# Optimization experiments

Hardware: AMD Instinct MI355X
Metric: run time of the kernel (lower is better)

The kernel has to match this reference:

```python
import jax, jax.numpy as jnp
import numpy as np

D = 256; DFFN = 1024; H = 8; NLVL = 4; NPNT = 4; HD = D // H
BS = 4; NQ = 100; NPTS = 25
SPATIAL = [(128, 128), (64, 64), (32, 32), (16, 16)]
LEN_IN = sum(h * w for h, w in SPATIAL)


def _ln(x, g, b, eps=1e-5):
    m = x.mean(-1, keepdims=True)
    v = ((x - m) ** 2).mean(-1, keepdims=True)
    return (x - m) * jax.lax.rsqrt(v + eps) * g + b


def _mha(q, k, v, w_in, b_in, w_out, b_out):
    # torch nn.MultiheadAttention math, batch-first layout [B,S,D]
    B, Sq, _ = q.shape; Sk = k.shape[1]
    wq, wk, wv = jnp.split(w_in, 3, 0); bq, bk, bv = jnp.split(b_in, 3)
    qh = (q @ wq.T + bq).reshape(B, Sq, H, HD).transpose(0, 2, 1, 3)
    kh = (k @ wk.T + bk).reshape(B, Sk, H, HD).transpose(0, 2, 1, 3)
    vh = (v @ wv.T + bv).reshape(B, Sk, H, HD).transpose(0, 2, 1, 3)
    a = jax.nn.softmax(jnp.einsum('bhqd,bhkd->bhqk', qh, kh) * (1.0 / float(np.sqrt(HD))), -1)
    o = jnp.einsum('bhqk,bhkd->bhqd', a, vh).transpose(0, 2, 1, 3).reshape(B, Sq, D)
    return o @ w_out.T + b_out


def _msdeform(query, ref, src, off_w, off_b, aw_w, aw_b, val_w, val_b, out_w, out_b):
    # MSDeformAttn: per-query multi-level bilinear sampling + weighted aggregation
    bs, Lq, _ = query.shape
    value = (src @ val_w.T + val_b).reshape(bs, LEN_IN, H, HD)
    off = (query @ off_w.T + off_b).reshape(bs, Lq, H, NLVL, NPNT, 2)
    aw = jax.nn.softmax((query @ aw_w.T + aw_b).reshape(bs, Lq, H, NLVL * NPNT), -1)
    aw = aw.reshape(bs, Lq, H, NLVL, NPNT)
    norm = jnp.array([[w, h] for h, w in SPATIAL], jnp.float32)  # (W,H) per level
    loc = ref[:, :, None, :, None, :] + off / norm[None, None, None, :, None, :]
    out = jnp.zeros((bs, H, Lq, HD), query.dtype)
    start = 0
    for l, (hh, ww) in enumerate(SPATIAL):
        v_l = value[:, start:start + hh * ww].transpose(0, 2, 1, 3)  # [bs,H,hw,HD]
        start += hh * ww
        # grid_sample align_corners=False pixel coords: loc*size - 0.5
        x = (loc[:, :, :, l, :, 0] * ww - 0.5).transpose(0, 2, 1, 3).reshape(bs, H, Lq * NPNT)
        y = (loc[:, :, :, l, :, 1] * hh - 0.5).transpose(0, 2, 1, 3).reshape(bs, H, Lq * NPNT)
        x0 = jnp.floor(x); y0 = jnp.floor(y); wx = x - x0; wy = y - y0
        x0i = x0.astype(jnp.int32); y0i = y0.astype(jnp.int32); x1i = x0i + 1; y1i = y0i + 1
        def g(xi, yi):
            valid = ((xi >= 0) & (xi < ww) & (yi >= 0) & (yi < hh)).astype(query.dtype)
            idx = jnp.clip(yi, 0, hh - 1) * ww + jnp.clip(xi, 0, ww - 1)
            return jnp.take_along_axis(v_l, idx[..., None], axis=2) * valid[..., None]
        s = (g(x0i, y0i) * ((1 - wx) * (1 - wy))[..., None]
             + g(x1i, y0i) * (wx * (1 - wy))[..., None]
             + g(x0i, y1i) * ((1 - wx) * wy)[..., None]
             + g(x1i, y1i) * (wx * wy)[..., None])
        s = s.reshape(bs, H, Lq, NPNT, HD)
        out = out + (s * aw[:, :, :, l].transpose(0, 2, 1, 3)[..., None]).sum(3)
    return out.transpose(0, 2, 1, 3).reshape(bs, Lq, D) @ out_w.T + out_b


def _fwd(tgt, query_pos, reference_points, src,
         w_in_intra, b_in_intra, w_out_intra, b_out_intra, g_norm_intra, b_norm_intra,
         w_in_inter, b_in_inter, w_out_inter, b_out_inter, g_norm_inter, b_norm_inter,
         off_w, off_b, aw_w, aw_b, val_w, val_b, co_w, co_b, g_norm_cross, b_norm_cross,
         lin1_w, lin1_b, lin2_w, lin2_b, g_norm3, b_norm3):
    bs, nq, npts, d = tgt.shape
    # intra-instance self-attention (over control points)
    q = (tgt + query_pos).reshape(bs * nq, npts, d)
    t2 = _mha(q, q, tgt.reshape(bs * nq, npts, d), w_in_intra, b_in_intra, w_out_intra, b_out_intra)
    tgt = _ln(tgt + t2.reshape(bs, nq, npts, d), g_norm_intra, b_norm_intra)
    # inter-instance self-attention (over queries), no pos embed per source code
    ti = tgt.transpose(0, 2, 1, 3).reshape(bs * npts, nq, d)
    t2 = _mha(ti, ti, ti, w_in_inter, b_in_inter, w_out_inter, b_out_inter)
    ti = _ln(ti + t2, g_norm_inter, b_norm_inter).reshape(bs, npts, nq, d).transpose(0, 2, 1, 3)
    # deformable cross-attention
    ref = jnp.broadcast_to(reference_points[:, :, None], (bs, nq, npts, NLVL, 2)).reshape(bs, nq * npts, NLVL, 2)
    qc = (ti + query_pos).reshape(bs, nq * npts, d)
    t2 = _msdeform(qc, ref, src, off_w, off_b, aw_w, aw_b, val_w, val_b, co_w, co_b).reshape(bs, nq, npts, d)
    tgt = _ln(ti + t2, g_norm_cross, b_norm_cross)
    # FFN
    ff = jax.nn.relu(tgt @ lin1_w.T + lin1_b) @ lin2_w.T + lin2_b
    return _ln(tgt + ff, g_norm3, b_norm3)


def setup_inputs() -> dict:
    key = jax.random.key(0)
    ki = iter(jax.random.split(key, 40))
    def rn(shape, sc=0.02):
        return jax.random.normal(next(ki), shape, jnp.float32) * sc
    inp = dict(
        tgt=jax.random.normal(next(ki), (BS, NQ, NPTS, D), jnp.float32),
        query_pos=jax.random.normal(next(ki), (BS, NQ, NPTS, D), jnp.float32),
        reference_points=jax.random.uniform(next(ki), (BS, NQ, NLVL, 2), jnp.float32),
        src=jax.random.normal(next(ki), (BS, LEN_IN, D), jnp.float32),
        w_in_intra=rn((3 * D, D)), b_in_intra=jnp.zeros((3 * D,), jnp.float32),
        w_out_intra=rn((D, D)), b_out_intra=jnp.zeros((D,), jnp.float32),
        g_norm_intra=jnp.ones((D,), jnp.float32), b_norm_intra=jnp.zeros((D,), jnp.float32),
        w_in_inter=rn((3 * D, D)), b_in_inter=jnp.zeros((3 * D,), jnp.float32),
        w_out_inter=rn((D, D)), b_out_inter=jnp.zeros((D,), jnp.float32),
        g_norm_inter=jnp.ones((D,), jnp.float32), b_norm_inter=jnp.zeros((D,), jnp.float32),
        off_w=rn((H * NLVL * NPNT * 2, D), 0.001), off_b=rn((H * NLVL * NPNT * 2,), 0.5),
        aw_w=rn((H * NLVL * NPNT, D)), aw_b=jnp.zeros((H * NLVL * NPNT,), jnp.float32),
        val_w=rn((D, D)), val_b=jnp.zeros((D,), jnp.float32),
        co_w=rn((D, D)), co_b=jnp.zeros((D,), jnp.float32),
        g_norm_cross=jnp.ones((D,), jnp.float32), b_norm_cross=jnp.zeros((D,), jnp.float32),
        lin1_w=rn((DFFN, D)), lin1_b=jnp.zeros((DFFN,), jnp.float32),
        lin2_w=rn((D, DFFN)), lin2_b=jnp.zeros((D,), jnp.float32),
        g_norm3=jnp.ones((D,), jnp.float32), b_norm3=jnp.zeros((D,), jnp.float32),
        src_spatial_shapes=jnp.array(SPATIAL, jnp.int32),
        level_start_index=jnp.array(np.cumsum([0] + [h * w for h, w in SPATIAL[:-1]]), jnp.int32),
    )
    return inp


def reference(tgt, query_pos, reference_points, src,
              w_in_intra, b_in_intra, w_out_intra, b_out_intra, g_norm_intra, b_norm_intra,
              w_in_inter, b_in_inter, w_out_inter, b_out_inter, g_norm_inter, b_norm_inter,
              off_w, off_b, aw_w, aw_b, val_w, val_b, co_w, co_b, g_norm_cross, b_norm_cross,
              lin1_w, lin1_b, lin2_w, lin2_b, g_norm3, b_norm3,
              src_spatial_shapes, level_start_index):
    # spatial shapes / level starts are compile-time constants (SPATIAL); args kept for signature parity
    return _fwd(tgt, query_pos, reference_points, src,
                w_in_intra, b_in_intra, w_out_intra, b_out_intra, g_norm_intra, b_norm_intra,
                w_in_inter, b_in_inter, w_out_inter, b_out_inter, g_norm_inter, b_norm_inter,
                off_w, off_b, aw_w, aw_b, val_w, val_b, co_w, co_b, g_norm_cross, b_norm_cross,
                lin1_w, lin1_b, lin2_w, lin2_b, g_norm3, b_norm3)
```

## Files before the change

### kernel.cpp

```cpp
#include <hip/hip_runtime.h>
#include <math.h>

#define DMODEL 256
#define HEADS  8
#define HDIM   32
#define BS     4
#define NQ     100
#define NPTS   25
#define LQ     2500
#define M10K   10000
#define LEN_IN 21760
#define MVAL   87040

typedef float f32x4 __attribute__((ext_vector_type(4)));
typedef short s16x8 __attribute__((ext_vector_type(8)));
typedef unsigned short u16;

static __device__ __forceinline__ short f2bf(float f) {
    unsigned u = __builtin_bit_cast(unsigned, f);
    u = (u + 0x7fffu + ((u >> 16) & 1u)) >> 16;
    return (short)u;
}
static __device__ __forceinline__ unsigned pack2(float lo, float hi) {
    return (unsigned)(u16)f2bf(lo) | ((unsigned)(u16)f2bf(hi) << 16);
}
static __device__ __forceinline__ float bf_lo(unsigned u) {
    return __builtin_bit_cast(float, u << 16);
}
static __device__ __forceinline__ float bf_hi(unsigned u) {
    return __builtin_bit_cast(float, u & 0xffff0000u);
}

#define LDSK   40
#define LDSK64 72

__global__ __launch_bounds__(256) void fat_stage0_kernel(
    const float* __restrict__ s0, const float* __restrict__ s1,
    const float* __restrict__ s2, const float* __restrict__ s3,
    const float* __restrict__ s4, const float* __restrict__ s5,
    const float* __restrict__ s6, const float* __restrict__ s7,
    const float* __restrict__ s8, const float* __restrict__ s9,
    u16* __restrict__ dst,
    const float* __restrict__ a, const float* __restrict__ b,
    u16* __restrict__ xb, u16* __restrict__ ab)
{
    if (blockIdx.x < 624) {
        int t8 = (blockIdx.x * 256 + threadIdx.x) * 8;
        if (t8 >= 1277952) return;
        const float* s; int base;
        if      (t8 <  196608) { s = s0; base = 0;       }
        else if (t8 <  262144) { s = s1; base = 196608;  }
        else if (t8 <  458752) { s = s2; base = 262144;  }
        else if (t8 <  524288) { s = s3; base = 458752;  }
        else if (t8 <  589824) { s = s4; base = 524288;  }
        else if (t8 <  622592) { s = s5; base = 589824;  }
        else if (t8 <  688128) { s = s6; base = 622592;  }
        else if (t8 <  753664) { s = s7; base = 688128;  }
        else if (t8 < 1015808) { s = s8; base = 753664;  }
        else                   { s = s9; base = 1015808; }
        const float* p = s + (t8 - base);
        float4 fa = *(const float4*)p;
        float4 fb = *(const float4*)(p + 4);
        s16x8 v;
        v[0]=f2bf(fa.x); v[1]=f2bf(fa.y); v[2]=f2bf(fa.z); v[3]=f2bf(fa.w);
        v[4]=f2bf(fb.x); v[5]=f2bf(fb.y); v[6]=f2bf(fb.z); v[7]=f2bf(fb.w);
        *(s16x8*)(dst + t8) = v;
    } else {
        int i = (blockIdx.x - 624) * 256 + threadIdx.x;
        size_t o = (size_t)i * 8;
        float4 a0 = *(const float4*)(a + o);
        float4 a1 = *(const float4*)(a + o + 4);
        s16x8 v;
        v[0]=f2bf(a0.x); v[1]=f2bf(a0.y); v[2]=f2bf(a0.z); v[3]=f2bf(a0.w);
        v[4]=f2bf(a1.x); v[5]=f2bf(a1.y); v[6]=f2bf(a1.z); v[7]=f2bf(a1.w);
        *(s16x8*)(ab + o) = v;
        float4 b0 = *(const float4*)(b + o);
        float4 b1 = *(const float4*)(b + o + 4);
        a0.x += b0.x; a0.y += b0.y; a0.z += b0.z; a0.w += b0.w;
        a1.x += b1.x; a1.y += b1.y; a1.z += b1.z; a1.w += b1.w;
        s16x8 w;
        w[0]=f2bf(a0.x); w[1]=f2bf(a0.y); w[2]=f2bf(a0.z); w[3]=f2bf(a0.w);
        w[4]=f2bf(a1.x); w[5]=f2bf(a1.y); w[6]=f2bf(a1.z); w[7]=f2bf(a1.w);
        *(s16x8*)(xb + o) = w;
    }
}


static __device__ __forceinline__ void body_value64(
    char* smem_, const float* __restrict__ A, const u16* __restrict__ W,
    const float* __restrict__ bias, u16* __restrict__ C, int bx, int by)
{
    short* As = (short*)smem_;
    short* Ws = (short*)(smem_ + 5120);

    const int tid = threadIdx.x;
    const int n0 = bx * 128;
    const int m0 = by * 64;

    const int arow = tid >> 2;
    const int ak = (tid & 3) * 8;
    const int wrow = tid >> 1;
    const int wk = (tid & 1) * 16;

    const float* aptr = A + (size_t)(m0 + arow) * 256 + ak;
    const u16* wptr = W + (size_t)(n0 + wrow) * 256 + wk;

    const int wave = tid >> 6;
    const int wm = wave & 1, wn = wave >> 1;
    const int lane = tid & 63;
    const int lrow = lane & 15, kq = lane >> 4;

    f32x4 acc[2][4];
#pragma unroll
    for (int i = 0; i < 2; ++i)
#pragma unroll
        for (int j = 0; j < 4; ++j) acc[i][j] = (f32x4)(0.f);

    float4 pa0 = *(const float4*)aptr;
    float4 pa1 = *(const float4*)(aptr + 4);
    s16x8 w0 = *(const s16x8*)wptr;
    s16x8 w1 = *(const s16x8*)(wptr + 8);

    for (int k0 = 0; k0 < 256; k0 += 32) {
        s16x8 av;
        av[0]=f2bf(pa0.x); av[1]=f2bf(pa0.y); av[2]=f2bf(pa0.z); av[3]=f2bf(pa0.w);
        av[4]=f2bf(pa1.x); av[5]=f2bf(pa1.y); av[6]=f2bf(pa1.z); av[7]=f2bf(pa1.w);
        *(s16x8*)&As[arow * LDSK + ak]     = av;
        *(s16x8*)&Ws[wrow * LDSK + wk]     = w0;
        *(s16x8*)&Ws[wrow * LDSK + wk + 8] = w1;
        __syncthreads();
        if (k0 + 32 < 256) {
            pa0 = *(const float4*)(aptr + k0 + 32);
            pa1 = *(const float4*)(aptr + k0 + 36);
            w0 = *(const s16x8*)(wptr + k0 + 32);
            w1 = *(const s16x8*)(wptr + k0 + 40);
        }

        s16x8 af[2], bfv[4];
#pragma unroll
        for (int i = 0; i < 2; ++i)
            af[i] = *(const s16x8*)&As[(wm * 32 + i * 16 + lrow) * LDSK + kq * 8];
#pragma unroll
        for (int j = 0; j < 4; ++j)
            bfv[j] = *(const s16x8*)&Ws[(wn * 64 + j * 16 + lrow) * LDSK + kq * 8];
#pragma unroll
        for (int i = 0; i < 2; ++i)
#pragma unroll
            for (int j = 0; j < 4; ++j)
                acc[i][j] = __builtin_amdgcn_mfma_f32_16x16x32_bf16(af[i], bfv[j], acc[i][j], 0, 0, 0);
        __syncthreads();
    }

#pragma unroll
    for (int i = 0; i < 2; ++i)
#pragma unroll
        for (int j = 0; j < 4; ++j) {
            int col = n0 + wn * 64 + j * 16 + lrow;
            float bv = bias[col];
#pragma unroll
            for (int reg = 0; reg < 4; ++reg) {
                int gmo = m0 + wm * 32 + i * 16 + kq * 4 + reg;
                C[(size_t)gmo * 256 + col] = (u16)f2bf(acc[i][j][reg] + bv);
            }
        }
}

static __device__ __forceinline__ void body_mfma128(
    char* smem_, const u16* __restrict__ A, const u16* __restrict__ W,
    const float* __restrict__ bias, u16* __restrict__ Cv, int bx, int by)
{
    short* As = (short*)smem_;
    short* Ws = (short*)(smem_ + 10240);

    const int tid = threadIdx.x;
    const int m0 = by * 128, n0 = bx * 128;
    const int srow = tid >> 1;
    const int sk = (tid & 1) * 16;
    const int wave = tid >> 6;
    const int wm = wave & 1, wn = wave >> 1;
    const int lane = tid & 63;
    const int lrow = lane & 15, kq = lane >> 4;

    const int gm = m0 + srow;
    const u16* aptr = A + (size_t)gm * 256 + sk;
    const u16* wptr = W + (size_t)(n0 + srow) * 256 + sk;

    f32x4 acc[4][4];
#pragma unroll
    for (int i = 0; i < 4; ++i)
#pragma unroll
        for (int j = 0; j < 4; ++j) acc[i][j] = (f32x4)(0.f);

    s16x8 a0 = (s16x8)0, a1 = (s16x8)0, w0, w1;
    if (gm < M10K) { a0 = *(const s16x8*)aptr; a1 = *(const s16x8*)(aptr + 8); }
    w0 = *(const s16x8*)wptr; w1 = *(const s16x8*)(wptr + 8);

    for (int k0 = 0; k0 < 256; k0 += 32) {
        *(s16x8*)&As[srow * LDSK + sk]     = a0;
        *(s16x8*)&As[srow * LDSK + sk + 8] = a1;
        *(s16x8*)&Ws[srow * LDSK + sk]     = w0;
        *(s16x8*)&Ws[srow * LDSK + sk + 8] = w1;
        __syncthreads();
        if (k0 + 32 < 256) {
            if (gm < M10K) {
                a0 = *(const s16x8*)(aptr + k0 + 32);
                a1 = *(const s16x8*)(aptr + k0 + 40);
            }
            w0 = *(const s16x8*)(wptr + k0 + 32);
            w1 = *(const s16x8*)(wptr + k0 + 40);
        }

        s16x8 af[4], bfv[4];
#pragma unroll
        for (int i = 0; i < 4; ++i)
            af[i] = *(const s16x8*)&As[(wm * 64 + i * 16 + lrow) * LDSK + kq * 8];
#pragma unroll
        for (int j = 0; j < 4; ++j)
            bfv[j] = *(const s16x8*)&Ws[(wn * 64 + j * 16 + lrow) * LDSK + kq * 8];
#pragma unroll
        for (int i = 0; i < 4; ++i)
#pragma unroll
            for (int j = 0; j < 4; ++j)
                acc[i][j] = __builtin_amdgcn_mfma_f32_16x16x32_bf16(af[i], bfv[j], acc[i][j], 0, 0, 0);
        __syncthreads();
    }

#pragma unroll
    for (int i = 0; i < 4; ++i)
#pragma unroll
        for (int j = 0; j < 4; ++j) {
            int col = n0 + wn * 64 + j * 16 + lrow;
            float bv = bias[col];
#pragma unroll
            for (int reg = 0; reg < 4; ++reg) {
                int gmo = m0 + wm * 64 + i * 16 + kq * 4 + reg;
                if (gmo < M10K)
                    Cv[(size_t)gmo * 768 + col] = (u16)f2bf(acc[i][j][reg] + bv);
            }
        }
}

static __device__ __forceinline__ void body_mfma64(
    char* smem_, const u16* __restrict__ A, const u16* __restrict__ W,
    const float* __restrict__ bias, u16* __restrict__ Cv, int bx, int by)
{
    short* As = (short*)smem_;
    short* Ws = (short*)(smem_ + 9216);

    const int tid = threadIdx.x;
    const int m0 = by * 64, n0 = bx * 64;
    const int srow = tid >> 2;
    const int sk = (tid & 3) * 16;
    const int wave = tid >> 6;
    const int wm = wave & 1, wn = wave >> 1;
    const int lane = tid & 63;
    const int lrow = lane & 15, kq = lane >> 4;

    const int gm = m0 + srow;
    const u16* aptr = A + (size_t)gm * 256 + sk;
    const u16* wptr = W + (size_t)(n0 + srow) * 256 + sk;

    f32x4 acc[2][2];
#pragma unroll
    for (int i = 0; i < 2; ++i)
#pragma unroll
        for (int j = 0; j < 2; ++j) acc[i][j] = (f32x4)(0.f);

    s16x8 a0 = (s16x8)0, a1 = (s16x8)0, w0, w1;
    if (gm < M10K) { a0 = *(const s16x8*)aptr; a1 = *(const s16x8*)(aptr + 8); }
    w0 = *(const s16x8*)wptr; w1 = *(const s16x8*)(wptr + 8);

    for (int k0 = 0; k0 < 256; k0 += 64) {
        *(s16x8*)&As[srow * LDSK64 + sk]     = a0;
        *(s16x8*)&As[srow * LDSK64 + sk + 8] = a1;
        *(s16x8*)&Ws[srow * LDSK64 + sk]     = w0;
        *(s16x8*)&Ws[srow * LDSK64 + sk + 8] = w1;
        __syncthreads();
        if (k0 + 64 < 256) {
            if (gm < M10K) {
                a0 = *(const s16x8*)(aptr + k0 + 64);
                a1 = *(const s16x8*)(aptr + k0 + 72);
            }
            w0 = *(const s16x8*)(wptr + k0 + 64);
            w1 = *(const s16x8*)(wptr + k0 + 72);
        }

#pragma unroll
        for (int s = 0; s < 2; ++s) {
            s16x8 af[2], bfv[2];
#pragma unroll
            for (int i = 0; i < 2; ++i)
                af[i] = *(const s16x8*)&As[(wm * 32 + i * 16 + lrow) * LDSK64 + s * 32 + kq * 8];
#pragma unroll
            for (int j = 0; j < 2; ++j)
                bfv[j] = *(const s16x8*)&Ws[(wn * 32 + j * 16 + lrow) * LDSK64 + s * 32 + kq * 8];
#pragma unroll
            for (int i = 0; i < 2; ++i)
#pragma unroll
                for (int j = 0; j < 2; ++j)
                    acc[i][j] = __builtin_amdgcn_mfma_f32_16x16x32_bf16(af[i], bfv[j], acc[i][j], 0, 0, 0);
        }
        __syncthreads();
    }

#pragma unroll
    for (int i = 0; i < 2; ++i)
#pragma unroll
        for (int j = 0; j < 2; ++j) {
            int col = n0 + wn * 32 + j * 16 + lrow;
            float bv = bias[col];
#pragma unroll
            for (int reg = 0; reg < 4; ++reg) {
                int gmo = m0 + wm * 32 + i * 16 + kq * 4 + reg;
                if (gmo < M10K)
                    Cv[(size_t)gmo * 768 + col] = (u16)f2bf(acc[i][j][reg] + bv);
            }
        }
}

__global__ __launch_bounds__(256) void fat_stage1_kernel(
    const float* __restrict__ src, const u16* __restrict__ wval,
    const float* __restrict__ valb, u16* __restrict__ valueb,
    const u16* __restrict__ x1b, const u16* __restrict__ wqk,
    const float* __restrict__ bqk, u16* __restrict__ qkvb,
    const u16* __restrict__ tgtb, const u16* __restrict__ wv,
    const float* __restrict__ bv, u16* __restrict__ qkvb_v)
{
    __shared__ __align__(16) char smem[20480];
    const int b = blockIdx.x;
    if (b < 2720) {
        body_value64(smem, src, wval, valb, valueb, b & 1, b >> 1);
    } else if (b < 3036) {
        const int bb = b - 2720;
        body_mfma128(smem, x1b, wqk, bqk, qkvb, bb & 3, bb >> 2);
    } else {
        const int bb = b - 3036;
        body_mfma64(smem, tgtb, wv, bv, qkvb_v, bb & 3, bb >> 2);
    }
}

__global__ __launch_bounds__(256) void gemm_mfma_kernel(
    const u16* __restrict__ A, int lda,
    const u16* __restrict__ W, int K,
    const float* __restrict__ bias,
    void* __restrict__ Cv, int ldc,
    int M, int relu, int out_bf16,
    int ncut, const float* __restrict__ bias2,
    float* __restrict__ Cv2, int ldc2)
{
    __shared__ short As[64 * LDSK64];
    __shared__ short Ws[64 * LDSK64];

    const int tid = threadIdx.x;
    const int m0 = blockIdx.y * 64, n0 = blockIdx.x * 64;
    const int srow = tid >> 2;
    const int sk = (tid & 3) * 16;
    const int wave = tid >> 6;
    const int wm = wave & 1, wn = wave >> 1;
    const int lane = tid & 63;
    const int lrow = lane & 15;
    const int kq = lane >> 4;

    const int gm = m0 + srow;
    const u16* aptr = A + (size_t)gm * lda + sk;
    const u16* wptr = W + (size_t)(n0 + srow) * K + sk;

    f32x4 acc[2][2];
#pragma unroll
    for (int i = 0; i < 2; ++i)
#pragma unroll
        for (int j = 0; j < 2; ++j) acc[i][j] = (f32x4)(0.f);

    s16x8 a0 = (s16x8)0, a1 = (s16x8)0, w0, w1;
    if (gm < M) { a0 = *(const s16x8*)aptr; a1 = *(const s16x8*)(aptr + 8); }
    w0 = *(const s16x8*)wptr; w1 = *(const s16x8*)(wptr + 8);

    for (int k0 = 0; k0 < K; k0 += 64) {
        *(s16x8*)&As[srow * LDSK64 + sk]     = a0;
        *(s16x8*)&As[srow * LDSK64 + sk + 8] = a1;
        *(s16x8*)&Ws[srow * LDSK64 + sk]     = w0;
        *(s16x8*)&Ws[srow * LDSK64 + sk + 8] = w1;
        __syncthreads();
        if (k0 + 64 < K) {
            if (gm < M) {
                a0 = *(const s16x8*)(aptr + k0 + 64);
                a1 = *(const s16x8*)(aptr + k0 + 72);
            }
            w0 = *(const s16x8*)(wptr + k0 + 64);
            w1 = *(const s16x8*)(wptr + k0 + 72);
        }

#pragma unroll
        for (int s = 0; s < 2; ++s) {
            s16x8 af[2], bfv[2];
#pragma unroll
            for (int i = 0; i < 2; ++i)
                af[i] = *(const s16x8*)&As[(wm * 32 + i * 16 + lrow) * LDSK64 + s * 32 + kq * 8];
#pragma unroll
            for (int j = 0; j < 2; ++j)
                bfv[j] = *(const s16x8*)&Ws[(wn * 32 + j * 16 + lrow) * LDSK64 + s * 32 + kq * 8];
#pragma unroll
            for (int i = 0; i < 2; ++i)
#pragma unroll
                for (int j = 0; j < 2; ++j)
                    acc[i][j] = __builtin_amdgcn_mfma_f32_16x16x32_bf16(af[i], bfv[j], acc[i][j], 0, 0, 0);
        }
        __syncthreads();
    }

#pragma unroll
    for (int i = 0; i < 2; ++i)
#pragma unroll
        for (int j = 0; j < 2; ++j) {
            int col = n0 + wn * 32 + j * 16 + lrow;
            float bv = (col < ncut) ? bias[col] : bias2[col - ncut];
#pragma unroll
            for (int reg = 0; reg < 4; ++reg) {
                int gmo = m0 + wm * 32 + i * 16 + kq * 4 + reg;
                if (gmo < M) {
                    float v = acc[i][j][reg] + bv;
                    if (relu) v = fmaxf(v, 0.f);
                    if (col < ncut) {
                        if (out_bf16)
                            ((u16*)Cv)[(size_t)gmo * ldc + col] = (u16)f2bf(v);
                        else
                            ((float*)Cv)[(size_t)gmo * ldc + col] = v;
                    } else {
                        Cv2[(size_t)gmo * ldc2 + (col - ncut)] = v;
                    }
                }
            }
        }
}

__global__ __launch_bounds__(256) void gemm_mfma128_kernel(
    const u16* __restrict__ A, int lda,
    const u16* __restrict__ W, int K,
    const float* __restrict__ bias,
    void* __restrict__ Cv, int ldc,
    int M, int relu, int out_bf16)
{
    __shared__ short As[128 * LDSK];
    __shared__ short Ws[128 * LDSK];

    const int tid = threadIdx.x;
    const int m0 = blockIdx.y * 128, n0 = blockIdx.x * 128;

    const int srow = tid >> 1;
    const int sk = (tid & 1) * 16;

    const int wave = tid >> 6;
    const int wm = wave & 1, wn = wave >> 1;
    const int lane = tid & 63;
    const int lrow = lane & 15;
    const int kq = lane >> 4;

    const int gm = m0 + srow;
    const u16* aptr = A + (size_t)gm * lda + sk;
    const u16* wptr = W + (size_t)(n0 + srow) * K + sk;

    f32x4 acc[4][4];
#pragma unroll
    for (int i = 0; i < 4; ++i)
#pragma unroll
        for (int j = 0; j < 4; ++j) acc[i][j] = (f32x4)(0.f);

    s16x8 a0 = (s16x8)0, a1 = (s16x8)0, w0, w1;
    if (gm < M) { a0 = *(const s16x8*)aptr; a1 = *(const s16x8*)(aptr + 8); }
    w0 = *(const s16x8*)wptr; w1 = *(const s16x8*)(wptr + 8);

    for (int k0 = 0; k0 < K; k0 += 32) {
        *(s16x8*)&As[srow * LDSK + sk]     = a0;
        *(s16x8*)&As[srow * LDSK + sk + 8] = a1;
        *(s16x8*)&Ws[srow * LDSK + sk]     = w0;
        *(s16x8*)&Ws[srow * LDSK + sk + 8] = w1;
        __syncthreads();
        if (k0 + 32 < K) {
            if (gm < M) {
                a0 = *(const s16x8*)(aptr + k0 + 32);
                a1 = *(const s16x8*)(aptr + k0 + 40);
            }
            w0 = *(const s16x8*)(wptr + k0 + 32);
            w1 = *(const s16x8*)(wptr + k0 + 40);
        }

        s16x8 af[4], bfv[4];
#pragma unroll
        for (int i = 0; i < 4; ++i)
            af[i] = *(const s16x8*)&As[(wm * 64 + i * 16 + lrow) * LDSK + kq * 8];
#pragma unroll
        for (int j = 0; j < 4; ++j)
            bfv[j] = *(const s16x8*)&Ws[(wn * 64 + j * 16 + lrow) * LDSK + kq * 8];
#pragma unroll
        for (int i = 0; i < 4; ++i)
#pragma unroll
            for (int j = 0; j < 4; ++j)
                acc[i][j] = __builtin_amdgcn_mfma_f32_16x16x32_bf16(af[i], bfv[j], acc[i][j], 0, 0, 0);
        __syncthreads();
    }

#pragma unroll
    for (int i = 0; i < 4; ++i)
#pragma unroll
        for (int j = 0; j < 4; ++j) {
            int col = n0 + wn * 64 + j * 16 + lrow;
            float bv = bias[col];
#pragma unroll
            for (int reg = 0; reg < 4; ++reg) {
                int gmo = m0 + wm * 64 + i * 16 + kq * 4 + reg;
                if (gmo < M) {
                    float v = acc[i][j][reg] + bv;
                    if (relu) v = fmaxf(v, 0.f);
                    if (out_bf16)
                        ((u16*)Cv)[(size_t)gmo * ldc + col] = (u16)f2bf(v);
                    else
                        ((float*)Cv)[(size_t)gmo * ldc + col] = v;
                }
            }
        }
}

__global__ __launch_bounds__(256) void inter_attn_mfma_kernel(
    const u16* __restrict__ qkv, u16* __restrict__ out, float scale)
{
    __shared__ __align__(16) u16 Qs[112 * 40];
    __shared__ __align__(16) u16 Ks[112 * 40];
    __shared__ __align__(16) u16 Vt[32 * 136];
    __shared__ __align__(16) u16 Ps[112 * 136];

    const int b = blockIdx.x, h = blockIdx.y;
    const u16* base = qkv + (size_t)b * 100 * 768;
    const int tid = threadIdx.x;
    const int wave = tid >> 6, lane = tid & 63;
    const int lr = lane & 15, quad = lane >> 4;

    for (int i = tid; i < 12 * 20; i += 256) {
        int row = 100 + i / 20, c = (i % 20) * 2;
        *(unsigned*)&Qs[row * 40 + c] = 0;
        *(unsigned*)&Ks[row * 40 + c] = 0;
    }
    for (int i = tid; i < 2176; i += 256) ((unsigned*)Vt)[i] = 0;
    for (int i = tid; i < 7616; i += 256) ((unsigned*)Ps)[i] = 0;
    __syncthreads();

    for (int idx = tid; idx < 2400; idx += 256) {
        int row = idx / 24, s = idx % 24;
        const u16* p = (s < 8)  ? base + row * 768 + h * 32 + s * 4
                     : (s < 16) ? base + row * 768 + 256 + h * 32 + (s - 8) * 4
                                : base + row * 768 + 512 + h * 32 + (s - 16) * 4;
        if (s < 8) {
            *(uint2*)&Qs[row * 40 + s * 4] = *(const uint2*)p;
        } else if (s < 16) {
            *(uint2*)&Ks[row * 40 + (s - 8) * 4] = *(const uint2*)p;
        } else {
            int d0 = (s - 16) * 4;
            Vt[(d0 + 0) * 136 + row] = p[0];
            Vt[(d0 + 1) * 136 + row] = p[1];
            Vt[(d0 + 2) * 136 + row] = p[2];
            Vt[(d0 + 3) * 136 + row] = p[3];
        }
    }
    __syncthreads();

#pragma unroll 1
    for (int rr = 0; rr < 2; ++rr) {
        int rt = wave + rr * 4;
        if (rt < 7) {
            s16x8 aq = *(const s16x8*)&Qs[(rt * 16 + lr) * 40 + quad * 8];
            f32x4 sc[7];
#pragma unroll
            for (int ct = 0; ct < 7; ++ct) {
                s16x8 bk = *(const s16x8*)&Ks[(ct * 16 + lr) * 40 + quad * 8];
                sc[ct] = __builtin_amdgcn_mfma_f32_16x16x32_bf16(aq, bk, (f32x4)(0.f), 0, 0, 0);
            }
            const bool colok[7] = {true, true, true, true, true, true, (lr < 4)};
#pragma unroll
            for (int reg = 0; reg < 4; ++reg) {
                float mx = -1e30f;
#pragma unroll
                for (int ct = 0; ct < 7; ++ct) {
                    float sv = sc[ct][reg] * scale;
                    sc[ct][reg] = sv;
                    if (colok[ct]) mx = fmaxf(mx, sv);
                }
#pragma unroll
                for (int d = 1; d < 16; d <<= 1) mx = fmaxf(mx, __shfl_xor(mx, d));
                float ssum = 0.f;
#pragma unroll
                for (int ct = 0; ct < 7; ++ct) {
                    float pv = colok[ct] ? __expf(sc[ct][reg] - mx) : 0.f;
                    sc[ct][reg] = pv;
                    ssum += pv;
                }
#pragma unroll
                for (int d = 1; d < 16; d <<= 1) ssum += __shfl_xor(ssum, d);
                float inv = 1.f / ssum;
                int prow = rt * 16 + quad * 4 + reg;
#pragma unroll
                for (int ct = 0; ct < 7; ++ct)
                    Ps[prow * 136 + ct * 16 + lr] = (u16)f2bf(sc[ct][reg] * inv);
            }
        }
    }
    __syncthreads();

#pragma unroll 1
    for (int rr = 0; rr < 2; ++rr) {
        int rt = wave + rr * 4;
        if (rt < 7) {
            f32x4 o0 = (f32x4)(0.f), o1 = (f32x4)(0.f);
#pragma unroll
            for (int kk = 0; kk < 4; ++kk) {
                s16x8 ap = *(const s16x8*)&Ps[(rt * 16 + lr) * 136 + kk * 32 + quad * 8];
                s16x8 bv0 = *(const s16x8*)&Vt[lr * 136 + kk * 32 + quad * 8];
                s16x8 bv1 = *(const s16x8*)&Vt[(16 + lr) * 136 + kk * 32 + quad * 8];
                o0 = __builtin_amdgcn_mfma_f32_16x16x32_bf16(ap, bv0, o0, 0, 0, 0);
                o1 = __builtin_amdgcn_mfma_f32_16x16x32_bf16(ap, bv1, o1, 0, 0, 0);
            }
#pragma unroll
            for (int reg = 0; reg < 4; ++reg) {
                int q = rt * 16 + quad * 4 + reg;
                if (q < 100) {
                    u16* op = out + ((size_t)b * 100 + q) * 256 + h * 32;
                    op[lr]      = (u16)f2bf(o0[reg]);
                    op[16 + lr] = (u16)f2bf(o1[reg]);
                }
            }
        }
    }
}

__global__ __launch_bounds__(256) void intra_fused_kernel(
    const u16* __restrict__ qkv,
    const u16* __restrict__ W,
    const float* __restrict__ bias,
    const float* __restrict__ res,
    const float* __restrict__ g, const float* __restrict__ beta,
    float* __restrict__ outf, u16* __restrict__ outbf,
    float scale)
{
    __shared__ __align__(16) uint2 KVh[25][128];
    __shared__ __align__(16) u16 Ao[32 * 264];
    __shared__ short Ws[256 * LDSK];
    __shared__ float redS[4][32];
    __shared__ float redV[4][32];

    const int inst = blockIdx.x;
    const int tid = threadIdx.x;
    const int h = tid >> 5, r = tid & 31;
    const u16* base = qkv + (size_t)inst * 25 * 768;
// ... 213 lines not shown
                              pack2(y.z + qv.z, y.w + qv.w));
        *(uint2*)(qout + oo) = pk;
    }
}

__global__ __launch_bounds__(256, 4) void msdeform_sample_kernel(
    const u16* __restrict__ value,
    const float* __restrict__ off,
    const float* __restrict__ awl,
    const float* __restrict__ refp,
    u16* __restrict__ sampled)
{
    const int unit = blockIdx.x * 8 + (threadIdx.x >> 5);
    const int t = threadIdx.x & 31;
    const int h = t >> 2, c8 = t & 3;
    const int b = unit / LQ, lq = unit - b * LQ;
    const int q = lq / NPTS;

    const float* awp = awl + (size_t)unit * 128 + h * 16;
    float w[16];
    float mx = -1e30f;
#pragma unroll
    for (int k = 0; k < 16; ++k) { w[k] = awp[k]; mx = fmaxf(mx, w[k]); }
    float sum = 0.f;
#pragma unroll
    for (int k = 0; k < 16; ++k) { w[k] = __expf(w[k] - mx); sum += w[k]; }
    const float inv = 1.f / sum;

    const float* offp = off + (size_t)unit * 256 + h * 32;
    const float* rp = refp + ((size_t)b * 100 + q) * 8;
    const u16* vbase = value + (size_t)b * LEN_IN * 256 + h * 32 + c8 * 8;

    float acc[8];
#pragma unroll
    for (int k = 0; k < 8; ++k) acc[k] = 0.f;

    int start = 0;
    const int sz[4] = {128, 64, 32, 16};
#pragma unroll
    for (int l = 0; l < 4; ++l) {
        const int hh = sz[l], ww = sz[l];
        const float rx = rp[l * 2 + 0], ry = rp[l * 2 + 1];
#pragma unroll 2
        for (int pt = 0; pt < 4; ++pt) {
            float ox = offp[(l * 4 + pt) * 2 + 0];
            float oy = offp[(l * 4 + pt) * 2 + 1];
            float x = rx * ww + ox - 0.5f;
            float y = ry * hh + oy - 0.5f;
            float x0f = floorf(x), y0f = floorf(y);
            float wx = x - x0f, wy = y - y0f;
            int x0 = (int)x0f, y0 = (int)y0f;
            int x1 = x0 + 1, y1 = y0 + 1;
            float aw = w[l * 4 + pt] * inv;

            int x0c = min(max(x0, 0), ww - 1), x1c = min(max(x1, 0), ww - 1);
            int y0c = min(max(y0, 0), hh - 1), y1c = min(max(y1, 0), hh - 1);
            float w00 = aw * (1.f - wx) * (1.f - wy);
            float w10 = aw * wx * (1.f - wy);
            float w01 = aw * (1.f - wx) * wy;
            float w11 = aw * wx * wy;
            if (!(x0 >= 0 && x0 < ww)) { w00 = 0.f; w01 = 0.f; }
            if (!(x1 >= 0 && x1 < ww)) { w10 = 0.f; w11 = 0.f; }
            if (!(y0 >= 0 && y0 < hh)) { w00 = 0.f; w10 = 0.f; }
            if (!(y1 >= 0 && y1 < hh)) { w01 = 0.f; w11 = 0.f; }

            uint4 u00 = *(const uint4*)(vbase + (size_t)(start + y0c * ww + x0c) * 256);
            uint4 u10 = *(const uint4*)(vbase + (size_t)(start + y0c * ww + x1c) * 256);
            uint4 u01 = *(const uint4*)(vbase + (size_t)(start + y1c * ww + x0c) * 256);
            uint4 u11 = *(const uint4*)(vbase + (size_t)(start + y1c * ww + x1c) * 256);

#define ACC4(u, wgt) \
            acc[0] = fmaf(wgt, bf_lo(u.x), acc[0]); \
            acc[1] = fmaf(wgt, bf_hi(u.x), acc[1]); \
            acc[2] = fmaf(wgt, bf_lo(u.y), acc[2]); \
            acc[3] = fmaf(wgt, bf_hi(u.y), acc[3]); \
            acc[4] = fmaf(wgt, bf_lo(u.z), acc[4]); \
            acc[5] = fmaf(wgt, bf_hi(u.z), acc[5]); \
            acc[6] = fmaf(wgt, bf_lo(u.w), acc[6]); \
            acc[7] = fmaf(wgt, bf_hi(u.w), acc[7]);
            ACC4(u00, w00); ACC4(u10, w10); ACC4(u01, w01); ACC4(u11, w11);
#undef ACC4
        }
        start += hh * ww;
    }

    uint4 pk;
    pk.x = pack2(acc[0], acc[1]); pk.y = pack2(acc[2], acc[3]);
    pk.z = pack2(acc[4], acc[5]); pk.w = pack2(acc[6], acc[7]);
    *(uint4*)(sampled + (size_t)unit * 256 + h * 32 + c8 * 8) = pk;
}

extern "C" void kernel_launch(void* const* d_in, const int* in_sizes, int n_in,
                              void* d_out, int out_size, void* d_ws, size_t ws_size,
                              hipStream_t stream)
{
    (void)in_sizes; (void)n_in; (void)out_size; (void)ws_size;

    const float* tgt        = (const float*)d_in[0];
    const float* query_pos  = (const float*)d_in[1];
    const float* refp       = (const float*)d_in[2];
    const float* src        = (const float*)d_in[3];
    const float* w_in_intra = (const float*)d_in[4];
    const float* b_in_intra = (const float*)d_in[5];
    const float* w_out_intra= (const float*)d_in[6];
    const float* b_out_intra= (const float*)d_in[7];
    const float* g_ln_intra = (const float*)d_in[8];
    const float* b_ln_intra = (const float*)d_in[9];
    const float* w_in_inter = (const float*)d_in[10];
    const float* b_in_inter = (const float*)d_in[11];
    const float* w_out_inter= (const float*)d_in[12];
    const float* b_out_inter= (const float*)d_in[13];
    const float* g_ln_inter = (const float*)d_in[14];
    const float* b_ln_inter = (const float*)d_in[15];
    const float* off_w      = (const float*)d_in[16];
    const float* off_b      = (const float*)d_in[17];
    const float* aw_w       = (const float*)d_in[18];
    const float* aw_b       = (const float*)d_in[19];
    const float* val_w      = (const float*)d_in[20];
    const float* val_b      = (const float*)d_in[21];
    const float* co_w       = (const float*)d_in[22];
    const float* co_b       = (const float*)d_in[23];
    const float* g_ln_cross = (const float*)d_in[24];
    const float* b_ln_cross = (const float*)d_in[25];
    const float* lin1_w     = (const float*)d_in[26];
    const float* lin1_b     = (const float*)d_in[27];
    const float* lin2_w     = (const float*)d_in[28];
    const float* lin2_b     = (const float*)d_in[29];
    const float* g_ln3      = (const float*)d_in[30];
    const float* b_ln3      = (const float*)d_in[31];

    float* ws    = (float*)d_ws;
    float* qkv   = ws;
    float* tmp   = ws + 7680000;
    u16*   attnb = (u16*)(ws + 10240000);
    float* tgt1  = ws + 11520000;
    float* ti    = ws + 14080000;
    u16*   tib   = (u16*)(ws + 16640000);
    float* tA    = ws + 17920000;
    u16*   qcb   = (u16*)(ws + 20480000);
    u16*   x1b   = (u16*)(ws + 21760000);
    u16*   tgtb  = (u16*)(ws + 23040000);
    float* awl   = ws + 24320000;
    u16*   valueb= (u16*)(ws + 25600000);
    u16*   wb    = (u16*)(ws + 36741120);
    float* out   = (float*)d_out;

    u16* qkvb = (u16*)qkv;

    u16* wb_in_intra  = wb;
    u16* wb_out_intra = wb + 196608;
    u16* wb_in_inter  = wb + 262144;
    u16* wb_out_inter = wb + 458752;
    u16* wb_off       = wb + 524288;
    u16* wb_val       = wb + 622592;
    u16* wb_co        = wb + 688128;
    u16* wb_lin1      = wb + 753664;
    u16* wb_lin2      = wb + 1015808;

    const float scale = 0.17677669529663687f;
    const int MB64  = (M10K + 63) / 64;
    const int MB128 = (M10K + 127) / 128;
    const int NC_OFF = 1 << 30;

    fat_stage0_kernel<<<1874, 256, 0, stream>>>(
        w_in_intra, w_out_intra, w_in_inter, w_out_inter, off_w,
        aw_w, val_w, co_w, lin1_w, lin2_w, wb,
        tgt, query_pos, x1b, tgtb);

    fat_stage1_kernel<<<3664, 256, 0, stream>>>(
        src, wb_val, val_b, valueb,
        x1b, wb_in_intra, b_in_intra, qkvb,
        tgtb, wb_in_intra + 512 * 256, b_in_intra + 512, qkvb + 512);

    intra_fused_kernel<<<400, 256, 0, stream>>>(qkvb, wb_out_intra, b_out_intra,
                                                tgt, g_ln_intra, b_ln_intra,
                                                ti, tib, scale);

    gemm_mfma128_kernel<<<dim3(6, MB128), 256, 0, stream>>>(tib, 256, wb_in_inter, 256,
                                                            b_in_inter, qkvb, 768, M10K, 0, 1);
    inter_attn_mfma_kernel<<<dim3(100, 8), 256, 0, stream>>>(qkvb, attnb, scale);
    gemm_mfma_kernel<<<dim3(4, MB64), 256, 0, stream>>>(attnb, 256, wb_out_inter, 256,
                                                        b_out_inter, tmp, 256, M10K, 0, 0,
                                                        NC_OFF, b_out_inter, (float*)0, 0);
    add_ln_kernel<<<2500, 256, 0, stream>>>(ti, tmp, g_ln_inter, b_ln_inter,
                                            tA, (u16*)0, query_pos, qcb, 1);

    gemm_mfma_kernel<<<dim3(6, MB64), 256, 0, stream>>>(qcb, 256, wb_off, 256,
                                                        off_b, tgt1, 256, M10K, 0, 0,
                                                        256, aw_b, awl, 128);
    msdeform_sample_kernel<<<1250, 256, 0, stream>>>(valueb, tgt1, awl, refp, attnb);
    gemm_mfma_kernel<<<dim3(4, MB64), 256, 0, stream>>>(attnb, 256, wb_co, 256,
                                                        co_b, tmp, 256, M10K, 0, 0,
                                                        NC_OFF, co_b, (float*)0, 0);
    add_ln_kernel<<<2500, 256, 0, stream>>>(tA, tmp, g_ln_cross, b_ln_cross,
                                            ti, tib, (const float*)0, (u16*)0, 0);

    gemm_mfma128_kernel<<<dim3(8, MB128), 256, 0, stream>>>(tib, 256, wb_lin1, 256,
                                                            lin1_b, valueb, 1024, M10K, 1, 1);
    gemm_mfma_kernel<<<dim3(4, MB64), 256, 0, stream>>>(valueb, 1024, wb_lin2, 1024,
                                                        lin2_b, tmp, 256, M10K, 0, 0,
                                                        NC_OFF, lin2_b, (float*)0, 0);
    add_ln_kernel<<<2500, 256, 0, stream>>>(ti, tmp, g_ln3, b_ln3,
                                            out, (u16*)0, (const float*)0, (u16*)0, 0);
}
```

Before: 456.1 us.

## Move value projection into stage0 using fp32 weights, widen gemm K-tile to 64

The value-projection GEMM now runs inside the first fused launch, reading fp32 weights directly and converting them in registers. It no longer waits for the weight-conversion pass or sits in the second launch, which shrinks stage1 and lets the large GEMM overlap with the conversion blocks. Separately, the 128x128 MFMA GEMM kernel stages 64-wide K tiles instead of 32, halving the number of barriers per K sweep. The cost is more LDS and register use per block, and extra fp32 weight reads and conversion in every value block.

```diff
diff --git a/kernel.cpp b/kernel.cpp
--- a/kernel.cpp
+++ b/kernel.cpp
@@ -34,6 +34,93 @@
 #define LDSK   40
 #define LDSK64 72
 
+static __device__ __forceinline__ void body_value64_wf32(
+    char* smem_, const float* __restrict__ A, const float* __restrict__ Wf,
+    const float* __restrict__ bias, u16* __restrict__ C, int bx, int by)
+{
+    short* As = (short*)smem_;
+    short* Ws = (short*)(smem_ + 5120);
+
+    const int tid = threadIdx.x;
+    const int n0 = bx * 128;
+    const int m0 = by * 64;
+
+    const int arow = tid >> 2;
+    const int ak = (tid & 3) * 8;
+    const int wrow = tid >> 1;
+    const int wk = (tid & 1) * 16;
+
+    const float* aptr = A + (size_t)(m0 + arow) * 256 + ak;
+    const float* wptr = Wf + (size_t)(n0 + wrow) * 256 + wk;
+
+    const int wave = tid >> 6;
+    const int wm = wave & 1, wn = wave >> 1;
+    const int lane = tid & 63;
+    const int lrow = lane & 15, kq = lane >> 4;
+
+    f32x4 acc[2][4];
+#pragma unroll
+    for (int i = 0; i < 2; ++i)
+#pragma unroll
+        for (int j = 0; j < 4; ++j) acc[i][j] = (f32x4)(0.f);
+
+    float4 pa0 = *(const float4*)aptr;
+    float4 pa1 = *(const float4*)(aptr + 4);
+    float4 pw0 = *(const float4*)(wptr);
+    float4 pw1 = *(const float4*)(wptr + 4);
+    float4 pw2 = *(const float4*)(wptr + 8);
+    float4 pw3 = *(const float4*)(wptr + 12);
+
+    for (int k0 = 0; k0 < 256; k0 += 32) {
+        s16x8 av, wv0, wv1;
+        av[0]=f2bf(pa0.x); av[1]=f2bf(pa0.y); av[2]=f2bf(pa0.z); av[3]=f2bf(pa0.w);
+        av[4]=f2bf(pa1.x); av[5]=f2bf(pa1.y); av[6]=f2bf(pa1.z); av[7]=f2bf(pa1.w);
+        wv0[0]=f2bf(pw0.x); wv0[1]=f2bf(pw0.y); wv0[2]=f2bf(pw0.z); wv0[3]=f2bf(pw0.w);
+        wv0[4]=f2bf(pw1.x); wv0[5]=f2bf(pw1.y); wv0[6]=f2bf(pw1.z); wv0[7]=f2bf(pw1.w);
+        wv1[0]=f2bf(pw2.x); wv1[1]=f2bf(pw2.y); wv1[2]=f2bf(pw2.z); wv1[3]=f2bf(pw2.w);
+        wv1[4]=f2bf(pw3.x); wv1[5]=f2bf(pw3.y); wv1[6]=f2bf(pw3.z); wv1[7]=f2bf(pw3.w);
+        *(s16x8*)&As[arow * LDSK + ak]     = av;
+        *(s16x8*)&Ws[wrow * LDSK + wk]     = wv0;
+        *(s16x8*)&Ws[wrow * LDSK + wk + 8] = wv1;
+        __syncthreads();
+        if (k0 + 32 < 256) {
+            pa0 = *(const float4*)(aptr + k0 + 32);
+            pa1 = *(const float4*)(aptr + k0 + 36);
+            pw0 = *(const float4*)(wptr + k0 + 32);
+            pw1 = *(const float4*)(wptr + k0 + 36);
+            pw2 = *(const float4*)(wptr + k0 + 40);
+            pw3 = *(const float4*)(wptr + k0 + 44);
+        }
+
+        s16x8 af[2], bfv[4];
+#pragma unroll
+        for (int i = 0; i < 2; ++i)
+            af[i] = *(const s16x8*)&As[(wm * 32 + i * 16 + lrow) * LDSK + kq * 8];
+#pragma unroll
+        for (int j = 0; j < 4; ++j)
+            bfv[j] = *(const s16x8*)&Ws[(wn * 64 + j * 16 + lrow) * LDSK + kq * 8];
+#pragma unroll
+        for (int i = 0; i < 2; ++i)
+#pragma unroll
+            for (int j = 0; j < 4; ++j)
+                acc[i][j] = __builtin_amdgcn_mfma_f32_16x16x32_bf16(af[i], bfv[j], acc[i][j], 0, 0, 0);
+        __syncthreads();
+    }
+
+#pragma unroll
+    for (int i = 0; i < 2; ++i)
+#pragma unroll
+        for (int j = 0; j < 4; ++j) {
+            int col = n0 + wn * 64 + j * 16 + lrow;
+            float bv = bias[col];
+#pragma unroll
+            for (int reg = 0; reg < 4; ++reg) {
+                int gmo = m0 + wm * 32 + i * 16 + kq * 4 + reg;
+                C[(size_t)gmo * 256 + col] = (u16)f2bf(acc[i][j][reg] + bv);
+            }
+        }
+}
+
 __global__ __launch_bounds__(256) void fat_stage0_kernel(
     const float* __restrict__ s0, const float* __restrict__ s1,
     const float* __restrict__ s2, const float* __restrict__ s3,
@@ -42,8 +129,11 @@
     const float* __restrict__ s8, const float* __restrict__ s9,
     u16* __restrict__ dst,
     const float* __restrict__ a, const float* __restrict__ b,
-    u16* __restrict__ xb, u16* __restrict__ ab)
-{
+    u16* __restrict__ xb, u16* __restrict__ ab,
+    const float* __restrict__ src, const float* __restrict__ valwf,
+    const float* __restrict__ valb, u16* __restrict__ valueb)
+{
+    __shared__ __align__(16) char smem0[15360];
     if (blockIdx.x < 624) {
         int t8 = (blockIdx.x * 256 + threadIdx.x) * 8;
         if (t8 >= 1277952) return;
@@ -65,7 +155,7 @@
         v[0]=f2bf(fa.x); v[1]=f2bf(fa.y); v[2]=f2bf(fa.z); v[3]=f2bf(fa.w);
         v[4]=f2bf(fb.x); v[5]=f2bf(fb.y); v[6]=f2bf(fb.z); v[7]=f2bf(fb.w);
         *(s16x8*)(dst + t8) = v;
-    } else {
+    } else if (blockIdx.x < 1874) {
         int i = (blockIdx.x - 624) * 256 + threadIdx.x;
         size_t o = (size_t)i * 8;
         float4 a0 = *(const float4*)(a + o);
@@ -82,88 +172,12 @@
         w[0]=f2bf(a0.x); w[1]=f2bf(a0.y); w[2]=f2bf(a0.z); w[3]=f2bf(a0.w);
         w[4]=f2bf(a1.x); w[5]=f2bf(a1.y); w[6]=f2bf(a1.z); w[7]=f2bf(a1.w);
         *(s16x8*)(xb + o) = w;
-    }
-}
-
-
-static __device__ __forceinline__ void body_value64(
-    char* smem_, const float* __restrict__ A, const u16* __restrict__ W,
-    const float* __restrict__ bias, u16* __restrict__ C, int bx, int by)
-{
-    short* As = (short*)smem_;
-    short* Ws = (short*)(smem_ + 5120);
-
-    const int tid = threadIdx.x;
-    const int n0 = bx * 128;
-    const int m0 = by * 64;
-
-    const int arow = tid >> 2;
-    const int ak = (tid & 3) * 8;
-    const int wrow = tid >> 1;
-    const int wk = (tid & 1) * 16;
-
-    const float* aptr = A + (size_t)(m0 + arow) * 256 + ak;
-    const u16* wptr = W + (size_t)(n0 + wrow) * 256 + wk;
-
-    const int wave = tid >> 6;
-    const int wm = wave & 1, wn = wave >> 1;
-    const int lane = tid & 63;
-    const int lrow = lane & 15, kq = lane >> 4;
-
-    f32x4 acc[2][4];
-#pragma unroll
-    for (int i = 0; i < 2; ++i)
-#pragma unroll
-        for (int j = 0; j < 4; ++j) acc[i][j] = (f32x4)(0.f);
-
-    float4 pa0 = *(const float4*)aptr;
-    float4 pa1 = *(const float4*)(aptr + 4);
-    s16x8 w0 = *(const s16x8*)wptr;
-    s16x8 w1 = *(const s16x8*)(wptr + 8);
-
-    for (int k0 = 0; k0 < 256; k0 += 32) {
-        s16x8 av;
-        av[0]=f2bf(pa0.x); av[1]=f2bf(pa0.y); av[2]=f2bf(pa0.z); av[3]=f2bf(pa0.w);
-        av[4]=f2bf(pa1.x); av[5]=f2bf(pa1.y); av[6]=f2bf(pa1.z); av[7]=f2bf(pa1.w);
-        *(s16x8*)&As[arow * LDSK + ak]     = av;
-        *(s16x8*)&Ws[wrow * LDSK + wk]     = w0;
-        *(s16x8*)&Ws[wrow * LDSK + wk + 8] = w1;
-        __syncthreads();
-        if (k0 + 32 < 256) {
-            pa0 = *(const float4*)(aptr + k0 + 32);
-            pa1 = *(const float4*)(aptr + k0 + 36);
-            w0 = *(const s16x8*)(wptr + k0 + 32);
-            w1 = *(const s16x8*)(wptr + k0 + 40);
-        }
-
-        s16x8 af[2], bfv[4];
-#pragma unroll
-        for (int i = 0; i < 2; ++i)
-            af[i] = *(const s16x8*)&As[(wm * 32 + i * 16 + lrow) * LDSK + kq * 8];
-#pragma unroll
-        for (int j = 0; j < 4; ++j)
-            bfv[j] = *(const s16x8*)&Ws[(wn * 64 + j * 16 + lrow) * LDSK + kq * 8];
-#pragma unroll
-        for (int i = 0; i < 2; ++i)
-#pragma unroll
-            for (int j = 0; j < 4; ++j)
-                acc[i][j] = __builtin_amdgcn_mfma_f32_16x16x32_bf16(af[i], bfv[j], acc[i][j], 0, 0, 0);
-        __syncthreads();
-    }
-
-#pragma unroll
-    for (int i = 0; i < 2; ++i)
-#pragma unroll
-        for (int j = 0; j < 4; ++j) {
-            int col = n0 + wn * 64 + j * 16 + lrow;
-            float bv = bias[col];
-#pragma unroll
-            for (int reg = 0; reg < 4; ++reg) {
-                int gmo = m0 + wm * 32 + i * 16 + kq * 4 + reg;
-                C[(size_t)gmo * 256 + col] = (u16)f2bf(acc[i][j][reg] + bv);
-            }
-        }
-}
+    } else {
+        const int vb = blockIdx.x - 1874;
+        body_value64_wf32(smem0, src, valwf, valb, valueb, vb & 1, vb >> 1);
+    }
+}
+
 
 static __device__ __forceinline__ void body_mfma128(
     char* smem_, const u16* __restrict__ A, const u16* __restrict__ W,
@@ -319,8 +333,6 @@
 }
 
 __global__ __launch_bounds__(256) void fat_stage1_kernel(
-    const float* __restrict__ src, const u16* __restrict__ wval,
-    const float* __restrict__ valb, u16* __restrict__ valueb,
     const u16* __restrict__ x1b, const u16* __restrict__ wqk,
     const float* __restrict__ bqk, u16* __restrict__ qkvb,
     const u16* __restrict__ tgtb, const u16* __restrict__ wv,
@@ -328,13 +340,10 @@
 {
     __shared__ __align__(16) char smem[20480];
     const int b = blockIdx.x;
-    if (b < 2720) {
-        body_value64(smem, src, wval, valb, valueb, b & 1, b >> 1);
-    } else if (b < 3036) {
-        const int bb = b - 2720;
-        body_mfma128(smem, x1b, wqk, bqk, qkvb, bb & 3, bb >> 2);
+    if (b < 316) {
+        body_mfma128(smem, x1b, wqk, bqk, qkvb, b & 3, b >> 2);
     } else {
-        const int bb = b - 3036;
+        const int bb = b - 316;
         body_mfma64(smem, tgtb, wv, bv, qkvb_v, bb & 3, bb >> 2);
     }
 }
@@ -440,14 +449,14 @@
     void* __restrict__ Cv, int ldc,
     int M, int relu, int out_bf16)
 {
-    __shared__ short As[128 * LDSK];
-    __shared__ short Ws[128 * LDSK];
+    __shared__ short As[128 * LDSK64];
+    __shared__ short Ws[128 * LDSK64];
 
     const int tid = threadIdx.x;
     const int m0 = blockIdx.y * 128, n0 = blockIdx.x * 128;
 
     const int srow = tid >> 1;
-    const int sk = (tid & 1) * 16;
+    const int sk = (tid & 1) * 32;
 
     const int wave = tid >> 6;
     const int wm = wave & 1, wn = wave >> 1;
@@ -465,37 +474,53 @@
 #pragma unroll
         for (int j = 0; j < 4; ++j) acc[i][j] = (f32x4)(0.f);
 
-    s16x8 a0 = (s16x8)0, a1 = (s16x8)0, w0, w1;
-    if (gm < M) { a0 = *(const s16x8*)aptr; a1 = *(const s16x8*)(aptr + 8); }
-    w0 = *(const s16x8*)wptr; w1 = *(const s16x8*)(wptr + 8);
-
-    for (int k0 = 0; k0 < K; k0 += 32) {
-        *(s16x8*)&As[srow * LDSK + sk]     = a0;
-        *(s16x8*)&As[srow * LDSK + sk + 8] = a1;
-        *(s16x8*)&Ws[srow * LDSK + sk]     = w0;
-        *(s16x8*)&Ws[srow * LDSK + sk + 8] = w1;
-        __syncthreads();
-        if (k0 + 32 < K) {
+    s16x8 a0 = (s16x8)0, a1 = (s16x8)0, a2 = (s16x8)0, a3 = (s16x8)0;
+    s16x8 w0, w1, w2, w3;
+    if (gm < M) {
+        a0 = *(const s16x8*)aptr;        a1 = *(const s16x8*)(aptr + 8);
+        a2 = *(const s16x8*)(aptr + 16); a3 = *(const s16x8*)(aptr + 24);
+    }
+    w0 = *(const s16x8*)wptr;        w1 = *(const s16x8*)(wptr + 8);
+    w2 = *(const s16x8*)(wptr + 16); w3 = *(const s16x8*)(wptr + 24);
+
+    for (int k0 = 0; k0 < K; k0 += 64) {
+        *(s16x8*)&As[srow * LDSK64 + sk]      = a0;
+        *(s16x8*)&As[srow * LDSK64 + sk + 8]  = a1;
+        *(s16x8*)&As[srow * LDSK64 + sk + 16] = a2;
+        *(s16x8*)&As[srow * LDSK64 + sk + 24] = a3;
+        *(s16x8*)&Ws[srow * LDSK64 + sk]      = w0;
+        *(s16x8*)&Ws[srow * LDSK64 + sk + 8]  = w1;
+        *(s16x8*)&Ws[srow * LDSK64 + sk + 16] = w2;
+        *(s16x8*)&Ws[srow * LDSK64 + sk + 24] = w3;
+        __syncthreads();
+        if (k0 + 64 < K) {
             if (gm < M) {
-                a0 = *(const s16x8*)(aptr + k0 + 32);
-                a1 = *(const s16x8*)(aptr + k0 + 40);
-            }
-            w0 = *(const s16x8*)(wptr + k0 + 32);
-            w1 = *(const s16x8*)(wptr + k0 + 40);
-        }
-
-        s16x8 af[4], bfv[4];
-#pragma unroll
-        for (int i = 0; i < 4; ++i)
-            af[i] = *(const s16x8*)&As[(wm * 64 + i * 16 + lrow) * LDSK + kq * 8];
-#pragma unroll
-        for (int j = 0; j < 4; ++j)
-            bfv[j] = *(const s16x8*)&Ws[(wn * 64 + j * 16 + lrow) * LDSK + kq * 8];
-#pragma unroll
-        for (int i = 0; i < 4; ++i)
+                a0 = *(const s16x8*)(aptr + k0 + 64);
+                a1 = *(const s16x8*)(aptr + k0 + 72);
+                a2 = *(const s16x8*)(aptr + k0 + 80);
+                a3 = *(const s16x8*)(aptr + k0 + 88);
+            }
+            w0 = *(const s16x8*)(wptr + k0 + 64);
+            w1 = *(const s16x8*)(wptr + k0 + 72);
+            w2 = *(const s16x8*)(wptr + k0 + 80);
+            w3 = *(const s16x8*)(wptr + k0 + 88);
+        }
+
+#pragma unroll
+        for (int s = 0; s < 2; ++s) {
+            s16x8 af[4], bfv[4];
+#pragma unroll
+            for (int i = 0; i < 4; ++i)
+                af[i] = *(const s16x8*)&As[(wm * 64 + i * 16 + lrow) * LDSK64 + s * 32 + kq * 8];
 #pragma unroll
             for (int j = 0; j < 4; ++j)
-                acc[i][j] = __builtin_amdgcn_mfma_f32_16x16x32_bf16(af[i], bfv[j], acc[i][j], 0, 0, 0);
+                bfv[j] = *(const s16x8*)&Ws[(wn * 64 + j * 16 + lrow) * LDSK64 + s * 32 + kq * 8];
+#pragma unroll
+            for (int i = 0; i < 4; ++i)
+#pragma unroll
+                for (int j = 0; j < 4; ++j)
+                    acc[i][j] = __builtin_amdgcn_mfma_f32_16x16x32_bf16(af[i], bfv[j], acc[i][j], 0, 0, 0);
+        }
         __syncthreads();
     }
 
@@ -1015,7 +1040,6 @@
     u16* wb_in_inter  = wb + 262144;
     u16* wb_out_inter = wb + 458752;
     u16* wb_off       = wb + 524288;
-    u16* wb_val       = wb + 622592;
     u16* wb_co        = wb + 688128;
     u16* wb_lin1      = wb + 753664;
     u16* wb_lin2      = wb + 1015808;
@@ -1025,13 +1049,13 @@
     const int MB128 = (M10K + 127) / 128;
     const int NC_OFF = 1 << 30;
 
-    fat_stage0_kernel<<<1874, 256, 0, stream>>>(
+    fat_stage0_kernel<<<4594, 256, 0, stream>>>(
         w_in_intra, w_out_intra, w_in_inter, w_out_inter, off_w,
         aw_w, val_w, co_w, lin1_w, lin2_w, wb,
-        tgt, query_pos, x1b, tgtb);
-
-    fat_stage1_kernel<<<3664, 256, 0, stream>>>(
-        src, wb_val, val_b, valueb,
+        tgt, query_pos, x1b, tgtb,
+        src, val_w, val_b, valueb);
+
+    fat_stage1_kernel<<<944, 256, 0, stream>>>(
         x1b, wb_in_intra, b_in_intra, qkvb,
         tgtb, wb_in_intra + 512 * 256, b_in_intra + 512, qkvb + 512);
 
```

New measurement: 454.5 us, median of 2. No clear change (-0.4%).
